# Kernel optimization log

Measured on AMD Instinct MI355X. Metric: run time of the kernel, lower is better.

Reference implementation:

```python
import jax, jax.numpy as jnp
import numpy as np

DIM = 192
HEADS = 6
EMB4 = 192  # embed_dim * 4

def layer_norm(x, g, b, eps=1e-5):
    mu = jnp.mean(x, axis=-1, keepdims=True)
    var = jnp.var(x, axis=-1, keepdims=True)
    return (x - mu) * jax.lax.rsqrt(var + eps) * g + b

def setup_inputs() -> dict:
    key = jax.random.key(0)
    ks = jax.random.split(key, 8)
    B, C, H, W = 4, DIM, 128, 128
    M = 256
    s = lambda fan: 1.0 / np.sqrt(fan)
    return {
        "x": jax.random.normal(ks[0], (B, C, H, W), jnp.float32),
        "prior": jax.random.normal(ks[1], (B, M, EMB4), jnp.float32),
        "ln1_g": jnp.ones((DIM,), jnp.float32),
        "ln1_b": jnp.zeros((DIM,), jnp.float32),
        "ln2_g": jnp.ones((EMB4,), jnp.float32),
        "ln2_b": jnp.zeros((EMB4,), jnp.float32),
        "Wq": jax.random.normal(ks[2], (DIM, DIM), jnp.float32) * s(DIM),
        "Wkv": jax.random.normal(ks[3], (EMB4, 2 * DIM), jnp.float32) * s(EMB4),
        "Wp": jax.random.normal(ks[4], (DIM, DIM), jnp.float32) * s(DIM),
        "bp": jnp.zeros((DIM,), jnp.float32),
    }

def reference(x, prior, ln1_g, ln1_b, ln2_g, ln2_b, Wq, Wkv, Wp, bp):
    B, C, H, W = x.shape
    nh = HEADS
    hd = C // nh
    scale = hd ** (-0.5)
    xt = x.reshape(B, C, H * W).transpose(0, 2, 1)  # b n c
    _x = layer_norm(xt, ln1_g, ln1_b)
    pr = layer_norm(prior, ln2_g, ln2_b)
    q = _x @ Wq                      # b n (h d)
    kv = pr @ Wkv                    # b m (2 h d)
    k, v = jnp.split(kv, 2, axis=-1)
    N = H * W
    Mlen = prior.shape[1]
    q = q.reshape(B, N, nh, hd).transpose(0, 2, 1, 3)      # b h n d
    k = k.reshape(B, Mlen, nh, hd).transpose(0, 2, 1, 3)   # b h m d
    v = v.reshape(B, Mlen, nh, hd).transpose(0, 2, 1, 3)   # b h m d
    attn = jnp.einsum('bhnd,bhmd->bhnm', q, k) * scale
    attn = jax.nn.softmax(attn, axis=-1)
    out = jnp.einsum('bhnm,bhmd->bhnd', attn, v)
    out = out.transpose(0, 2, 1, 3).reshape(B, N, C)
    out = out @ Wp + bp
    y = xt + out
    return y.transpose(0, 2, 1).reshape(B, C, H, W)
```

## Files before the change

### kernel.cpp

```cpp
#include <hip/hip_runtime.h>

typedef unsigned short u16;
typedef unsigned int u32;

#define C_DIM 192
#define N_TOK 16384
#define M_LEN 256
#define HD 32
#define NH 6

#define AF_STRIDE 3080

typedef __attribute__((ext_vector_type(8))) short short8v;
typedef __attribute__((ext_vector_type(4))) float float4v;

__device__ __forceinline__ u32 cvt_pk_bf16(float lo, float hi) {
    u32 r;
    asm("v_cvt_pk_bf16_f32 %0, %1, %2" : "=v"(r) : "v"(lo), "v"(hi));
    return r;
}
__device__ __forceinline__ u16 f2bf_hw(float f) {
    return (u16)cvt_pk_bf16(f, f);
}

__device__ __forceinline__ void wprep_frag(
    const float* __restrict__ W, u16* __restrict__ outp, int gt)
{
    int f = gt >> 6, lane = gt & 63;
    int q8 = lane >> 4, ln = lane & 15;
    int wv = f / 18, r = f % 18;
    int kt = r / 3, jj = r % 3;
    const float* w0 = W + (kt * 32 + q8 * 8) * C_DIM + (wv * 3 + jj) * 16 + ln;
    union { u32 w[4]; short8v v; } out;
#pragma unroll
    for (int j = 0; j < 4; ++j)
        out.w[j] = cvt_pk_bf16(w0[(2 * j) * C_DIM], w0[(2 * j + 1) * C_DIM]);
    *(short8v*)&outp[f * 512 + lane * 8] = out.v;
}

__global__ __launch_bounds__(256) void w_prep2(
    const float* __restrict__ Wq, u16* __restrict__ WqF,
    const float* __restrict__ Wp, u16* __restrict__ WpF)
{
    int bb = blockIdx.x;
    const float* W = (bb < 18) ? Wq : Wp;
    u16* outp = (bb < 18) ? WqF : WpF;
    wprep_frag(W, outp, (bb % 18) * 256 + threadIdx.x);
}

__global__ __launch_bounds__(192) void ln2_kv_wprep(
    const float* __restrict__ prior, const float* __restrict__ g,
    const float* __restrict__ beta, const float* __restrict__ Wkv,
    u16* __restrict__ KfG, u16* __restrict__ VfG,
    const float* __restrict__ Wq, u16* __restrict__ WqF,
    const float* __restrict__ Wp, u16* __restrict__ WpF)
{
    int tid = threadIdx.x;
    if (blockIdx.x >= 1024) {
        int bb = blockIdx.x - 1024;
        const float* W = (bb < 24) ? Wq : Wp;
        u16* outp = (bb < 24) ? WqF : WpF;
        wprep_frag(W, outp, (bb % 24) * 192 + tid);
        return;
    }
    __shared__ float pr[C_DIM];
    __shared__ float red[3][2];
    int row = blockIdx.x;
    int wv = tid >> 6;
    float val = prior[row * C_DIM + tid];
    float s1 = val, s2 = val * val;
#pragma unroll
    for (int m = 1; m < 64; m <<= 1) {
        s1 += __shfl_xor(s1, m);
        s2 += __shfl_xor(s2, m);
    }
    if ((tid & 63) == 0) { red[wv][0] = s1; red[wv][1] = s2; }
    __syncthreads();
    float a  = red[0][0] + red[1][0] + red[2][0];
    float c2 = red[0][1] + red[1][1] + red[2][1];
    float mu = a * (1.f / C_DIM);
    float rs = rsqrtf(c2 * (1.f / C_DIM) - mu * mu + 1e-5f);
    pr[tid] = (val - mu) * rs * g[tid] + beta[tid];
    __syncthreads();
    float ka = 0.f, va = 0.f;
    for (int c = 0; c < C_DIM; ++c) {
        float p = pr[c];
        ka += p * Wkv[c * 384 + tid];
        va += p * Wkv[c * 384 + 192 + tid];
    }
    int b = row >> 8, m = row & 255;
    int h = tid >> 5, dim = tid & 31;
    int bh = b * NH + h;
    int kt = m >> 4, r = m & 15;
    {
        int qd = dim >> 3, j = dim & 7;
        KfG[bh * 8192 + kt * 512 + (qd * 16 + r) * 8 + j] =
            f2bf_hw(ka * 0.17677669529663687f);
    }
    {
        int qd = r >> 2, reg = r & 3;
        int P = kt >> 1;
        int j = reg + 4 * (kt & 1);
        int dh = dim >> 4, n = dim & 15;
        VfG[bh * 8192 + (P * 2 + dh) * 512 + (qd * 16 + n) * 8 + j] = f2bf_hw(va);
    }
}

__global__ __launch_bounds__(256) void ln1_q_mfma(
    const float* __restrict__ x, const float* __restrict__ g,
    const float* __restrict__ beta, const u16* __restrict__ WqF,
    u16* __restrict__ q)
{
    __shared__ u16 Af[4 * AF_STRIDE];
    __shared__ u16 Tq[64 * 200];
    __shared__ float part[64][4][2];
    __shared__ float mu_s[64], rs_s[64];
    int b = blockIdx.x >> 8;
    int n0 = (blockIdx.x & 255) * 64;
    int t = threadIdx.x;
    int wv = t >> 6, lane = t & 63;

    float xv[48];
    {
        const float* xb = x + (((size_t)(b * C_DIM + wv * 48)) << 14) + n0 + lane;
        float s1p[4] = {0,0,0,0}, s2p[4] = {0,0,0,0};
#pragma unroll
        for (int i = 0; i < 48; ++i) {
            float f = xb[(size_t)i << 14];
            xv[i] = f;
            s1p[i & 3] += f;
            s2p[i & 3] += f * f;
        }
        part[lane][wv][0] = (s1p[0] + s1p[1]) + (s1p[2] + s1p[3]);
        part[lane][wv][1] = (s2p[0] + s2p[1]) + (s2p[2] + s2p[3]);
    }
    __syncthreads();
    if (t < 64) {
        float a  = part[t][0][0] + part[t][1][0] + part[t][2][0] + part[t][3][0];
        float c2 = part[t][0][1] + part[t][1][1] + part[t][2][1] + part[t][3][1];
        float mu = a * (1.f / C_DIM);
        mu_s[t] = mu;
        rs_s[t] = rsqrtf(c2 * (1.f / C_DIM) - mu * mu + 1e-5f);
    }
    __syncthreads();

    {
        float mu = mu_s[lane], rs = rs_s[lane];
        int mt2 = lane >> 4, ln2 = lane & 15;
        u32* A32 = (u32*)Af;
#pragma unroll
        for (int i = 0; i < 48; i += 2) {
            int c = wv * 48 + i;
            float f0 = (xv[i]     - mu) * rs * g[c]     + beta[c];
            float f1 = (xv[i + 1] - mu) * rs * g[c + 1] + beta[c + 1];
            int kt = c >> 5, k8 = (c & 31) >> 3, j = c & 7;
            A32[(mt2 * AF_STRIDE + kt * 512 + k8 * 128 + ln2 * 8 + j) >> 1] =
                cvt_pk_bf16(f0, f1);
        }
    }
    __syncthreads();

    int q8 = lane >> 4, ln = lane & 15;
    short8v Bf[18];
#pragma unroll
    for (int i = 0; i < 18; ++i)
        Bf[i] = *(const short8v*)&WqF[(wv * 18 + i) * 512 + lane * 8];

#pragma unroll
    for (int mt = 0; mt < 4; ++mt) {
        float4v acc[3] = {{0.f,0.f,0.f,0.f},{0.f,0.f,0.f,0.f},{0.f,0.f,0.f,0.f}};
#pragma unroll
        for (int kt = 0; kt < 6; ++kt) {
            short8v a = *(const short8v*)&Af[mt * AF_STRIDE + kt * 512 + lane * 8];
#pragma unroll
            for (int jj = 0; jj < 3; ++jj)
                acc[jj] = __builtin_amdgcn_mfma_f32_16x16x32_bf16(a, Bf[kt * 3 + jj], acc[jj], 0, 0, 0);
        }
#pragma unroll
        for (int jj = 0; jj < 3; ++jj)
#pragma unroll
            for (int r = 0; r < 4; ++r)
                Tq[(mt * 16 + q8 * 4 + r) * 200 + (wv * 3 + jj) * 16 + ln] = f2bf_hw(acc[jj][r]);
    }
    __syncthreads();

    {
        int tok = t >> 2, pp = t & 3;
        const uint4* src = (const uint4*)&Tq[tok * 200 + pp * 48];
        uint4* dst = (uint4*)(q + ((size_t)(b * N_TOK + n0 + tok)) * C_DIM + pp * 48);
#pragma unroll
        for (int i = 0; i < 6; ++i) dst[i] = src[i];
    }
}

__global__ __launch_bounds__(192) void ln2_kv_frag(
    const float* __restrict__ prior, const float* __restrict__ g,
    const float* __restrict__ beta, const float* __restrict__ Wkv,
    u16* __restrict__ KfG, u16* __restrict__ VfG)
{
    __shared__ float pr[C_DIM];
    __shared__ float red[3][2];
    int row = blockIdx.x;
    int tid = threadIdx.x;
    int wv = tid >> 6;
    float val = prior[row * C_DIM + tid];
    float s1 = val, s2 = val * val;
#pragma unroll
    for (int m = 1; m < 64; m <<= 1) {
        s1 += __shfl_xor(s1, m);
        s2 += __shfl_xor(s2, m);
    }
    if ((tid & 63) == 0) { red[wv][0] = s1; red[wv][1] = s2; }
    __syncthreads();
    float a  = red[0][0] + red[1][0] + red[2][0];
    float c2 = red[0][1] + red[1][1] + red[2][1];
    float mu = a * (1.f / C_DIM);
    float rs = rsqrtf(c2 * (1.f / C_DIM) - mu * mu + 1e-5f);
    pr[tid] = (val - mu) * rs * g[tid] + beta[tid];
    __syncthreads();
    float ka = 0.f, va = 0.f;
    for (int c = 0; c < C_DIM; ++c) {
        float p = pr[c];
        ka += p * Wkv[c * 384 + tid];
        va += p * Wkv[c * 384 + 192 + tid];
    }
    int b = row >> 8, m = row & 255;
    int h = tid >> 5, dim = tid & 31;
    int bh = b * NH + h;
    int kt = m >> 4, r = m & 15;
    {
        int qd = dim >> 3, j = dim & 7;
        KfG[bh * 8192 + kt * 512 + (qd * 16 + r) * 8 + j] =
            f2bf_hw(ka * 0.17677669529663687f);
    }
    {
        int qd = r >> 2, reg = r & 3;
        int P = kt >> 1;
        int j = reg + 4 * (kt & 1);
        int dh = dim >> 4, n = dim & 15;
        VfG[bh * 8192 + (P * 2 + dh) * 512 + (qd * 16 + n) * 8 + j] = f2bf_hw(va);
    }
}

__global__ __launch_bounds__(384, 2) void attn_proj_fused(
    const u16* __restrict__ q, const u16* __restrict__ KfG,
    const u16* __restrict__ VfG, const u16* __restrict__ WpF,
    const float* __restrict__ bp, const float* __restrict__ x,
    float* __restrict__ y)
{
    __shared__ float Tf[C_DIM * 68];
    u16* att_lds = (u16*)Tf;
    int b  = blockIdx.x >> 8;
    int n0 = (blockIdx.x & 255) * 64;
    int t = threadIdx.x;
    int wave = t >> 6, lane = t & 63;
    int quad = lane >> 4, ln = lane & 15;
    const float LOG2E = 1.4426950408889634f;

    int h = wave;
    short8v k_r[16], v_r[16];
    {
        const u16* Kf = KfG + (b * NH + h) * 8192;
        const u16* Vf = VfG + (b * NH + h) * 8192;
#pragma unroll
        for (int kt = 0; kt < 16; ++kt)
            k_r[kt] = *(const short8v*)&Kf[kt * 512 + lane * 8];
#pragma unroll
        for (int kt = 0; kt < 16; ++kt)
            v_r[kt] = *(const short8v*)&Vf[kt * 512 + lane * 8];
    }

    {
        const u16* qbase = q + ((size_t)(b * N_TOK + n0 + ln)) * C_DIM + h * HD + quad * 8;
        short8v qnext = *(const short8v*)qbase;

        for (int rep = 0; rep < 4; ++rep) {
            short8v qf = qnext;
            int nrep = rep < 3 ? rep + 1 : 3;
            qnext = *(const short8v*)(qbase + (size_t)nrep * 16 * C_DIM);

            float4v s[16];
#pragma unroll
            for (int kt = 0; kt < 16; ++kt) {
                float4v z = {0.f, 0.f, 0.f, 0.f};
                s[kt] = __builtin_amdgcn_mfma_f32_16x16x32_bf16(k_r[kt], qf, z, 0, 0, 0);
            }

            float mx = fmaxf(fmaxf(s[0][0], s[0][1]), fmaxf(s[0][2], s[0][3]));
#pragma unroll
            for (int kt = 1; kt < 16; ++kt)
                mx = fmaxf(fmaxf(mx, s[kt][0]),
                           fmaxf(s[kt][1], fmaxf(s[kt][2], s[kt][3])));
            mx = fmaxf(mx, __shfl_xor(mx, 16));
            mx = fmaxf(mx, __shfl_xor(mx, 32));

            float nm = -mx * LOG2E;
            float l = 0.f;
#pragma unroll
            for (int kt = 0; kt < 16; ++kt) {
#pragma unroll
                for (int r = 0; r < 4; ++r) {
                    float p = __builtin_amdgcn_exp2f(fmaf(s[kt][r], LOG2E, nm));
                    s[kt][r] = p;
                    l += p;
                }
            }
            l += __shfl_xor(l, 16);
            l += __shfl_xor(l, 32);
            float inv = __builtin_amdgcn_rcpf(l);

            float4v o0 = {0.f, 0.f, 0.f, 0.f}, o1 = {0.f, 0.f, 0.f, 0.f};
#pragma unroll
            for (int P = 0; P < 8; ++P) {
                union { u32 w[4]; short8v v; } pf;
                pf.w[0] = cvt_pk_bf16(s[2 * P][0],     s[2 * P][1]);
                pf.w[1] = cvt_pk_bf16(s[2 * P][2],     s[2 * P][3]);
                pf.w[2] = cvt_pk_bf16(s[2 * P + 1][0], s[2 * P + 1][1]);
                pf.w[3] = cvt_pk_bf16(s[2 * P + 1][2], s[2 * P + 1][3]);
                o0 = __builtin_amdgcn_mfma_f32_16x16x32_bf16(pf.v, v_r[2 * P],     o0, 0, 0, 0);
                o1 = __builtin_amdgcn_mfma_f32_16x16x32_bf16(pf.v, v_r[2 * P + 1], o1, 0, 0, 0);
            }

#pragma unroll
            for (int r = 0; r < 4; ++r) {
                float invr = __shfl(inv, quad * 4 + r);
                u16* rw = &att_lds[(rep * 16 + quad * 4 + r) * 200 + h * HD];
                rw[ln]      = f2bf_hw(o0[r] * invr);
                rw[16 + ln] = f2bf_hw(o1[r] * invr);
            }
        }
    }
    __syncthreads();

    float4 xu[8];
    {
        int r0 = t >> 4, p = t & 15;
#pragma unroll
        for (int pass = 0; pass < 8; ++pass) {
            int c = pass * 24 + r0;
            xu[pass] = ((const float4*)(x + (((size_t)(b * C_DIM + c)) << 14) + n0))[p];
        }
    }

    short8v Bf[12];
#pragma unroll
    for (int jc = 0; jc < 2; ++jc) {
        int cf = wave * 2 + jc;
        int wv = cf / 3, jj = cf % 3;
#pragma unroll
        for (int kt = 0; kt < 6; ++kt)
            Bf[jc * 6 + kt] = *(const short8v*)&WpF[(wv * 18 + kt * 3 + jj) * 512 + lane * 8];
    }

    float4v acc[4][2];
#pragma unroll
    for (int mt = 0; mt < 4; ++mt) {
#pragma unroll
        for (int jc = 0; jc < 2; ++jc) {
            float4v z = {0.f, 0.f, 0.f, 0.f};
            acc[mt][jc] = z;
        }
#pragma unroll
        for (int kt = 0; kt < 6; ++kt) {
            short8v a = *(const short8v*)&att_lds[(mt * 16 + ln) * 200 + quad * 8 + kt * 32];
#pragma unroll
            for (int jc = 0; jc < 2; ++jc)
                acc[mt][jc] = __builtin_amdgcn_mfma_f32_16x16x32_bf16(a, Bf[jc * 6 + kt], acc[mt][jc], 0, 0, 0);
        }
    }
    __syncthreads();

#pragma unroll
    for (int mt = 0; mt < 4; ++mt)
#pragma unroll
        for (int jc = 0; jc < 2; ++jc) {
            int c = (wave * 2 + jc) * 16 + ln;
#pragma unroll
            for (int r = 0; r < 4; ++r)
                Tf[c * 68 + mt * 16 + quad * 4 + r] = acc[mt][jc][r];
        }
    __syncthreads();

    {
        int r0 = t >> 4;
        int p  = t & 15;
#pragma unroll
        for (int pass = 0; pass < 8; ++pass) {
            int c = pass * 24 + r0;
            float bias = bp[c];
            float4 a = *(const float4*)&Tf[c * 68 + p * 4];
            float4*       yr = (float4*)(y + (((size_t)(b * C_DIM + c)) << 14) + n0);
            float4 u = xu[pass];
            float4 w;
            w.x = a.x + bias + u.x;
            w.y = a.y + bias + u.y;
            w.z = a.z + bias + u.z;
            w.w = a.w + bias + u.w;
            yr[p] = w;
        }
    }
}

__global__ __launch_bounds__(256) void attn_mfma_kernel(
    const u16* __restrict__ q, const u16* __restrict__ KfG,
    const u16* __restrict__ VfG, u16* __restrict__ att)
{
    __shared__ u16 sh[16384];
    int tb = blockIdx.x & 63;
    int bh = blockIdx.x >> 6;
    int h = bh % NH, b = bh / NH;
    int tid = threadIdx.x;
    int wave = tid >> 6, lane = tid & 63;
    int quad = lane >> 4, ln = lane & 15;

    const u16* qbase = q + ((size_t)(b * N_TOK + tb * 256 + wave * 16 + ln)) * C_DIM
                         + h * HD + quad * 8;
    short8v qnext = *(const short8v*)qbase;

    {
        const uint4* Ks = (const uint4*)(KfG + bh * 8192);
        const uint4* Vs = (const uint4*)(VfG + bh * 8192);
        uint4* d = (uint4*)sh;
#pragma unroll
        for (int i = tid; i < 2048; i += 256)
            d[i] = (i < 1024) ? Ks[i] : Vs[i - 1024];
    }
    __syncthreads();

    const u16* Kf = sh;
    const u16* Vf = sh + 8192;
    const float LOG2E = 1.4426950408889634f;

    for (int rep = 0; rep < 4; ++rep) {
        short8v qf = qnext;
        int nrep = rep < 3 ? rep + 1 : 3;
        qnext = *(const short8v*)(qbase + (size_t)nrep * 64 * C_DIM);

        float4v s[16];
#pragma unroll
        for (int kt = 0; kt < 16; ++kt) {
            short8v kf = *(const short8v*)&Kf[kt * 512 + lane * 8];
            float4v z = {0.f, 0.f, 0.f, 0.f};
            s[kt] = __builtin_amdgcn_mfma_f32_16x16x32_bf16(kf, qf, z, 0, 0, 0);
        }

        float mx = fmaxf(fmaxf(s[0][0], s[0][1]), fmaxf(s[0][2], s[0][3]));
#pragma unroll
        for (int kt = 1; kt < 16; ++kt)
            mx = fmaxf(fmaxf(mx, s[kt][0]),
                       fmaxf(s[kt][1], fmaxf(s[kt][2], s[kt][3])));
        mx = fmaxf(mx, __shfl_xor(mx, 16));
        mx = fmaxf(mx, __shfl_xor(mx, 32));

        float nm = -mx * LOG2E;
        float l = 0.f;
#pragma unroll
        for (int kt = 0; kt < 16; ++kt) {
#pragma unroll
            for (int r = 0; r < 4; ++r) {
                float p = __builtin_amdgcn_exp2f(fmaf(s[kt][r], LOG2E, nm));
                s[kt][r] = p;
                l += p;
            }
        }
        l += __shfl_xor(l, 16);
        l += __shfl_xor(l, 32);
        float inv = __builtin_amdgcn_rcpf(l);

        float4v o0 = {0.f, 0.f, 0.f, 0.f}, o1 = {0.f, 0.f, 0.f, 0.f};
#pragma unroll
        for (int P = 0; P < 8; ++P) {
            union { u32 w[4]; short8v v; } pf;
            pf.w[0] = cvt_pk_bf16(s[2 * P][0],     s[2 * P][1]);
            pf.w[1] = cvt_pk_bf16(s[2 * P][2],     s[2 * P][3]);
            pf.w[2] = cvt_pk_bf16(s[2 * P + 1][0], s[2 * P + 1][1]);
            pf.w[3] = cvt_pk_bf16(s[2 * P + 1][2], s[2 * P + 1][3]);
            short8v v0 = *(const short8v*)&Vf[(P * 2 + 0) * 512 + lane * 8];
            short8v v1 = *(const short8v*)&Vf[(P * 2 + 1) * 512 + lane * 8];
            o0 = __builtin_amdgcn_mfma_f32_16x16x32_bf16(pf.v, v0, o0, 0, 0, 0);
            o1 = __builtin_amdgcn_mfma_f32_16x16x32_bf16(pf.v, v1, o1, 0, 0, 0);
        }

        int token0 = tb * 256 + rep * 64 + wave * 16;
#pragma unroll
        for (int r = 0; r < 4; ++r) {
            float invr = __shfl(inv, quad * 4 + r);
            u16* row = att + ((size_t)(b * N_TOK + token0 + quad * 4 + r)) * C_DIM + h * HD;
            row[ln]      = f2bf_hw(o0[r] * invr);
            row[16 + ln] = f2bf_hw(o1[r] * invr);
        }
    }
}

__global__ __launch_bounds__(256) void proj_res_mfma(
    const u16* __restrict__ att, const float* __restrict__ Wp,
    const u16* __restrict__ WpF, const float* __restrict__ bp,
    const float* __restrict__ x, float* __restrict__ y)
{
    __shared__ float Tf[C_DIM * 68];
    int b = blockIdx.x >> 8;
    int n0 = (blockIdx.x & 255) * 64;
    int t = threadIdx.x;
    int wv = t >> 6, lane = t & 63;
    int q8 = lane >> 4, ln = lane & 15;

    short8v Bf[18];
    if (WpF) {
#pragma unroll
        for (int i = 0; i < 18; ++i)
            Bf[i] = *(const short8v*)&WpF[(wv * 18 + i) * 512 + lane * 8];
    } else {
#pragma unroll
        for (int kt = 0; kt < 6; ++kt) {
#pragma unroll
            for (int jj = 0; jj < 3; ++jj) {
                const float* w0 = Wp + (kt * 32 + q8 * 8) * C_DIM + (wv * 3 + jj) * 16 + ln;
                union { u32 w[4]; short8v v; } f;
#pragma unroll
                for (int wj = 0; wj < 4; ++wj)
                    f.w[wj] = cvt_pk_bf16(w0[(2 * wj) * C_DIM], w0[(2 * wj + 1) * C_DIM]);
                Bf[kt * 3 + jj] = f.v;
            }
        }
    }

#pragma unroll
    for (int mt = 0; mt < 4; ++mt) {
        const u16* ab = att + ((size_t)(b * N_TOK + n0 + mt * 16 + ln)) * C_DIM + q8 * 8;
        float4v acc[3] = {{0.f,0.f,0.f,0.f},{0.f,0.f,0.f,0.f},{0.f,0.f,0.f,0.f}};
#pragma unroll
        for (int kt = 0; kt < 6; ++kt) {
            short8v a = *(const short8v*)(ab + kt * 32);
#pragma unroll
            for (int jj = 0; jj < 3; ++jj)
                acc[jj] = __builtin_amdgcn_mfma_f32_16x16x32_bf16(a, Bf[kt * 3 + jj], acc[jj], 0, 0, 0);
        }
#pragma unroll
        for (int jj = 0; jj < 3; ++jj)
#pragma unroll
            for (int r = 0; r < 4; ++r)
                Tf[((wv * 3 + jj) * 16 + ln) * 68 + mt * 16 + q8 * 4 + r] = acc[jj][r];
    }
    __syncthreads();

    {
        int r0 = t >> 4;
        int p  = t & 15;
#pragma unroll
        for (int pass = 0; pass < 12; ++pass) {
            int c = pass * 16 + r0;
            float bias = bp[c];
            float4 a = *(const float4*)&Tf[c * 68 + p * 4];
            const float4* xr = (const float4*)(x + (((size_t)(b * C_DIM + c)) << 14) + n0);
            float4*       yr = (float4*)(y + (((size_t)(b * C_DIM + c)) << 14) + n0);
            float4 u = xr[p];
            float4 w;
            w.x = a.x + bias + u.x;
            w.y = a.y + bias + u.y;
            w.z = a.z + bias + u.z;
            w.w = a.w + bias + u.w;
            yr[p] = w;
        }
    }
}

extern "C" void kernel_launch(void* const* d_in, const int* in_sizes, int n_in,
                              void* d_out, int out_size, void* d_ws, size_t ws_size,
                              hipStream_t stream) {
    const float* x     = (const float*)d_in[0];
    const float* prior = (const float*)d_in[1];
    const float* ln1_g = (const float*)d_in[2];
    const float* ln1_b = (const float*)d_in[3];
    const float* ln2_g = (const float*)d_in[4];
    const float* ln2_b = (const float*)d_in[5];
    const float* Wq    = (const float*)d_in[6];
    const float* Wkv   = (const float*)d_in[7];
    const float* Wp    = (const float*)d_in[8];
    const float* bp    = (const float*)d_in[9];

    char* outc = (char*)d_out;
    float* y = (float*)d_out;

    const size_t needF = 25165824ull + 393216ull * 2 + 73728ull * 2;
    if (ws_size >= needF) {
        char* wsc = (char*)d_ws;
        u16* qb  = (u16*)wsc;
        u16* KfG = (u16*)(wsc + 25165824);
        u16* VfG = (u16*)(wsc + 25165824 + 393216);
        u16* WqF = (u16*)(wsc + 25165824 + 786432);
        u16* WpF = (u16*)(wsc + 25165824 + 786432 + 73728);

        ln2_kv_wprep<<<1072, 192, 0, stream>>>(
            prior, ln2_g, ln2_b, Wkv, KfG, VfG, Wq, WqF, Wp, WpF);
        ln1_q_mfma<<<1024, 256, 0, stream>>>(x, ln1_g, ln1_b, WqF, qb);
        attn_proj_fused<<<1024, 384, 0, stream>>>(qb, KfG, VfG, WpF, bp, x, y);
    } else {
        u16*   qb   = (u16*)outc;
        u16*   WqF  = (u16*)(outc + 26738688);
        u16*   KfG  = (u16*)(outc + 26812416);
        u16*   VfG  = (u16*)(outc + 27205632);
        u16*   att  = (u16*)d_ws;
        bool has_wpf = ws_size >= 25165824ull + 73728ull;
        u16* WpF = has_wpf ? (u16*)((char*)d_ws + 25165824) : (u16*)nullptr;

        w_prep2<<<has_wpf ? 36 : 18, 256, 0, stream>>>(Wq, WqF, Wp, has_wpf ? WpF : WqF);
        ln1_q_mfma<<<1024, 256, 0, stream>>>(x, ln1_g, ln1_b, WqF, qb);
        ln2_kv_frag<<<1024, 192, 0, stream>>>(prior, ln2_g, ln2_b, Wkv, KfG, VfG);
        attn_mfma_kernel<<<1536, 256, 0, stream>>>(qb, KfG, VfG, att);
        proj_res_mfma<<<1024, 256, 0, stream>>>(att, Wp, WpF, bp, x, y);
    }
}
```

Before: 186.4 us.

## Merge LN2/KV projection and LN1/Q projection into one interleaved kernel

Moves weight fragment prep into a small w_prep2 launch and fuses the prior LayerNorm+KV projection with the x LayerNorm+Q MFMA projection into one 2048-block kernel, alternating odd/even blocks. The aim is to let the tiny KV work overlap with the bandwidth-bound Q path and to remove a serialized launch boundary. In exchange, KV blocks now reserve the full Q-path shared memory and 256 threads with 64 of them idle, which can lower occupancy. A separate tiny launch is also still needed before the merged kernel.

After: 189.5 us. Within noise of the previous version (+1.7%).

```diff
diff --git a/kernel.cpp b/kernel.cpp
--- a/kernel.cpp
+++ b/kernel.cpp
@@ -48,61 +48,150 @@
     wprep_frag(W, outp, (bb % 18) * 256 + threadIdx.x);
 }
 
-__global__ __launch_bounds__(192) void ln2_kv_wprep(
-    const float* __restrict__ prior, const float* __restrict__ g,
-    const float* __restrict__ beta, const float* __restrict__ Wkv,
-    u16* __restrict__ KfG, u16* __restrict__ VfG,
-    const float* __restrict__ Wq, u16* __restrict__ WqF,
-    const float* __restrict__ Wp, u16* __restrict__ WpF)
+__global__ __launch_bounds__(256) void ln_merged(
+    const float* __restrict__ x, const float* __restrict__ g1,
+    const float* __restrict__ b1, const u16* __restrict__ WqF,
+    u16* __restrict__ q,
+    const float* __restrict__ prior, const float* __restrict__ g2,
+    const float* __restrict__ b2, const float* __restrict__ Wkv,
+    u16* __restrict__ KfG, u16* __restrict__ VfG)
 {
-    int tid = threadIdx.x;
-    if (blockIdx.x >= 1024) {
-        int bb = blockIdx.x - 1024;
-        const float* W = (bb < 24) ? Wq : Wp;
-        u16* outp = (bb < 24) ? WqF : WpF;
-        wprep_frag(W, outp, (bb % 24) * 192 + tid);
+    __shared__ u16 Af[4 * AF_STRIDE];
+    __shared__ u16 Tq[64 * 200];
+    __shared__ float part[64][4][2];
+    __shared__ float mu_s[64], rs_s[64];
+    int t = threadIdx.x;
+
+    if (blockIdx.x & 1) {
+        float* pr  = &part[0][0][0];
+        float* red = pr + 192;
+        int row = blockIdx.x >> 1;
+        int wv = t >> 6;
+        float val = 0.f, s1 = 0.f, s2 = 0.f;
+        if (t < 192) {
+            val = prior[row * C_DIM + t];
+            s1 = val; s2 = val * val;
+        }
+#pragma unroll
+        for (int m = 1; m < 64; m <<= 1) {
+            s1 += __shfl_xor(s1, m);
+            s2 += __shfl_xor(s2, m);
+        }
+        if (t < 192 && (t & 63) == 0) { red[wv * 2] = s1; red[wv * 2 + 1] = s2; }
+        __syncthreads();
+        float mu = 0.f, rs = 0.f;
+        if (t < 192) {
+            float a  = red[0] + red[2] + red[4];
+            float c2 = red[1] + red[3] + red[5];
+            mu = a * (1.f / C_DIM);
+            rs = rsqrtf(c2 * (1.f / C_DIM) - mu * mu + 1e-5f);
+        }
+        __syncthreads();
+        if (t < 192)
+            pr[t] = (val - mu) * rs * g2[t] + b2[t];
+        __syncthreads();
+        if (t < 192) {
+            float ka = 0.f, va = 0.f;
+            for (int c = 0; c < C_DIM; ++c) {
+                float p = pr[c];
+                ka += p * Wkv[c * 384 + t];
+                va += p * Wkv[c * 384 + 192 + t];
+            }
+            int b = row >> 8, m = row & 255;
+            int h = t >> 5, dim = t & 31;
+            int bh = b * NH + h;
+            int kt = m >> 4, r = m & 15;
+            {
+                int qd = dim >> 3, j = dim & 7;
+                KfG[bh * 8192 + kt * 512 + (qd * 16 + r) * 8 + j] =
+                    f2bf_hw(ka * 0.17677669529663687f);
+            }
+            {
+                int qd = r >> 2, reg = r & 3;
+                int P = kt >> 1;
+                int j = reg + 4 * (kt & 1);
+                int dh = dim >> 4, n = dim & 15;
+                VfG[bh * 8192 + (P * 2 + dh) * 512 + (qd * 16 + n) * 8 + j] = f2bf_hw(va);
+            }
+        }
         return;
     }
-    __shared__ float pr[C_DIM];
-    __shared__ float red[3][2];
-    int row = blockIdx.x;
-    int wv = tid >> 6;
-    float val = prior[row * C_DIM + tid];
-    float s1 = val, s2 = val * val;
-#pragma unroll
-    for (int m = 1; m < 64; m <<= 1) {
-        s1 += __shfl_xor(s1, m);
-        s2 += __shfl_xor(s2, m);
-    }
-    if ((tid & 63) == 0) { red[wv][0] = s1; red[wv][1] = s2; }
-    __syncthreads();
-    float a  = red[0][0] + red[1][0] + red[2][0];
-    float c2 = red[0][1] + red[1][1] + red[2][1];
-    float mu = a * (1.f / C_DIM);
-    float rs = rsqrtf(c2 * (1.f / C_DIM) - mu * mu + 1e-5f);
-    pr[tid] = (val - mu) * rs * g[tid] + beta[tid];
-    __syncthreads();
-    float ka = 0.f, va = 0.f;
-    for (int c = 0; c < C_DIM; ++c) {
-        float p = pr[c];
-        ka += p * Wkv[c * 384 + tid];
-        va += p * Wkv[c * 384 + 192 + tid];
-    }
-    int b = row >> 8, m = row & 255;
-    int h = tid >> 5, dim = tid & 31;
-    int bh = b * NH + h;
-    int kt = m >> 4, r = m & 15;
-    {
-        int qd = dim >> 3, j = dim & 7;
-        KfG[bh * 8192 + kt * 512 + (qd * 16 + r) * 8 + j] =
-            f2bf_hw(ka * 0.17677669529663687f);
-    }
-    {
-        int qd = r >> 2, reg = r & 3;
-        int P = kt >> 1;
-        int j = reg + 4 * (kt & 1);
-        int dh = dim >> 4, n = dim & 15;
-        VfG[bh * 8192 + (P * 2 + dh) * 512 + (qd * 16 + n) * 8 + j] = f2bf_hw(va);
+
+    int tile = blockIdx.x >> 1;
+    int b = tile >> 8;
+    int n0 = (tile & 255) * 64;
+    int wv = t >> 6, lane = t & 63;
+
+    float xv[48];
+    {
+        const float* xb = x + (((size_t)(b * C_DIM + wv * 48)) << 14) + n0 + lane;
+        float s1p[4] = {0,0,0,0}, s2p[4] = {0,0,0,0};
+#pragma unroll
+        for (int i = 0; i < 48; ++i) {
+            float f = xb[(size_t)i << 14];
+            xv[i] = f;
+            s1p[i & 3] += f;
+            s2p[i & 3] += f * f;
+        }
+        part[lane][wv][0] = (s1p[0] + s1p[1]) + (s1p[2] + s1p[3]);
+        part[lane][wv][1] = (s2p[0] + s2p[1]) + (s2p[2] + s2p[3]);
+    }
+    __syncthreads();
+    if (t < 64) {
+        float a  = part[t][0][0] + part[t][1][0] + part[t][2][0] + part[t][3][0];
+        float c2 = part[t][0][1] + part[t][1][1] + part[t][2][1] + part[t][3][1];
+        float mu = a * (1.f / C_DIM);
+        mu_s[t] = mu;
+        rs_s[t] = rsqrtf(c2 * (1.f / C_DIM) - mu * mu + 1e-5f);
+    }
+    __syncthreads();
+
+    {
+        float mu = mu_s[lane], rs = rs_s[lane];
+        int mt2 = lane >> 4, ln2 = lane & 15;
+        u32* A32 = (u32*)Af;
+#pragma unroll
+        for (int i = 0; i < 48; i += 2) {
+            int c = wv * 48 + i;
+            float f0 = (xv[i]     - mu) * rs * g1[c]     + b1[c];
+            float f1 = (xv[i + 1] - mu) * rs * g1[c + 1] + b1[c + 1];
+            int kt = c >> 5, k8 = (c & 31) >> 3, j = c & 7;
+            A32[(mt2 * AF_STRIDE + kt * 512 + k8 * 128 + ln2 * 8 + j) >> 1] =
+                cvt_pk_bf16(f0, f1);
+        }
+    }
+    __syncthreads();
+
+    int q8 = lane >> 4, ln = lane & 15;
+    short8v Bf[18];
+#pragma unroll
+    for (int i = 0; i < 18; ++i)
+        Bf[i] = *(const short8v*)&WqF[(wv * 18 + i) * 512 + lane * 8];
+
+#pragma unroll
+    for (int mt = 0; mt < 4; ++mt) {
+        float4v acc[3] = {{0.f,0.f,0.f,0.f},{0.f,0.f,0.f,0.f},{0.f,0.f,0.f,0.f}};
+#pragma unroll
+        for (int kt = 0; kt < 6; ++kt) {
+            short8v a = *(const short8v*)&Af[mt * AF_STRIDE + kt * 512 + lane * 8];
+#pragma unroll
+            for (int jj = 0; jj < 3; ++jj)
+                acc[jj] = __builtin_amdgcn_mfma_f32_16x16x32_bf16(a, Bf[kt * 3 + jj], acc[jj], 0, 0, 0);
+        }
+#pragma unroll
+        for (int jj = 0; jj < 3; ++jj)
+#pragma unroll
+            for (int r = 0; r < 4; ++r)
+                Tq[(mt * 16 + q8 * 4 + r) * 200 + (wv * 3 + jj) * 16 + ln] = f2bf_hw(acc[jj][r]);
+    }
+    __syncthreads();
+
+    {
+        int tok = t >> 2, pp = t & 3;
+        const uint4* src = (const uint4*)&Tq[tok * 200 + pp * 48];
+        uint4* dst = (uint4*)(q + ((size_t)(b * N_TOK + n0 + tok)) * C_DIM + pp * 48);
+#pragma unroll
+        for (int i = 0; i < 6; ++i) dst[i] = src[i];
     }
 }
 
@@ -590,9 +679,10 @@
         u16* WqF = (u16*)(wsc + 25165824 + 786432);
         u16* WpF = (u16*)(wsc + 25165824 + 786432 + 73728);
 
-        ln2_kv_wprep<<<1072, 192, 0, stream>>>(
-            prior, ln2_g, ln2_b, Wkv, KfG, VfG, Wq, WqF, Wp, WpF);
-        ln1_q_mfma<<<1024, 256, 0, stream>>>(x, ln1_g, ln1_b, WqF, qb);
+        w_prep2<<<36, 256, 0, stream>>>(Wq, WqF, Wp, WpF);
+        ln_merged<<<2048, 256, 0, stream>>>(
+            x, ln1_g, ln1_b, WqF, qb,
+            prior, ln2_g, ln2_b, Wkv, KfG, VfG);
         attn_proj_fused<<<1024, 384, 0, stream>>>(qb, KfG, VfG, WpF, bp, x, y);
     } else {
         u16*   qb   = (u16*)outc;
```
